# Kernel optimization log

Measured on AMD Instinct MI355X. Metric: run time of the kernel, lower is better.

## Reference

```python
import jax, jax.numpy as jnp
import numpy as np

B, T, D = 64, 4096, 100   # batch, tokens, token_dim == code_dim
K = 4                     # discrete_size: codebook entries
BETA = 0.25               # commitment loss weight


def setup_inputs() -> dict:
    key = jax.random.key(0)
    k_x, k_w, k_b, k_c = jax.random.split(key, 4)
    x = jax.random.normal(k_x, (B, T, D), dtype=jnp.float32)
    W1 = jax.random.normal(k_w, (D, D), dtype=jnp.float32) * (1.0 / np.sqrt(D))
    b1 = jax.random.normal(k_b, (D,), dtype=jnp.float32) * 0.01
    codebook = jax.random.normal(k_c, (K, D), dtype=jnp.float32)
    return {"x": x, "W1": W1, "b1": b1, "codebook": codebook, "quantize": 1}


def reference(x, W1, b1, codebook, quantize):
    # Linear1: Linear(100,100) + ReLU (torch Linear: x @ W.T + b)
    h = jax.nn.relu(jnp.einsum("btd,ed->bte", x, W1) + b1)  # [B,T,D]
    if not quantize:
        return (h, 0, 0, 0)
    # quantizer.compress: VQ-style cdist/argmin/straight-through/loss
    flat = h.reshape(-1, D)  # [N,D]
    d2 = (jnp.sum(flat * flat, axis=-1, keepdims=True)
          - 2.0 * flat @ codebook.T
          + jnp.sum(codebook * codebook, axis=-1))
    idx = jnp.argmin(d2, axis=-1)          # [N] nearest code indices
    q = codebook[idx]                       # [N,D] gathered codes
    sg = jax.lax.stop_gradient
    # codebook loss + commitment loss
    vq_loss = (jnp.mean((sg(flat) - q) ** 2)
               + BETA * jnp.mean((flat - sg(q)) ** 2))
    # straight-through quantized output
    aux = (flat + sg(q - flat)).reshape(B, T, D)
    payload = idx.reshape(B, T)
    return (h, payload, aux, vq_loss)
```

## Files before the change

kernel.cpp:

```cpp
#include <hip/hip_runtime.h>

#define D_DIM   100
#define K_CODES 4
#define RPB     64
#define TPB     256
#define PITCH   65
#define N_ROWS  262144
#define KP      128
#define NP      128
#define TAU     0.25

typedef __attribute__((ext_vector_type(8))) __bf16 bf16x8;
typedef __attribute__((ext_vector_type(4))) float  f32x4;

__device__ __forceinline__ unsigned short f2bf_rne(float f) {
    unsigned int u = __builtin_bit_cast(unsigned int, f);
    unsigned int r = u + 0x7fffu + ((u >> 16) & 1u);
    return (unsigned short)(r >> 16);
}
__device__ __forceinline__ float bf2f(unsigned short b) {
    unsigned int u = ((unsigned int)b) << 16;
    return __builtin_bit_cast(float, u);
}

__device__ __forceinline__ void load_lds16(const float* g, float* s) {
    __builtin_amdgcn_global_load_lds(
        (const __attribute__((address_space(1))) unsigned int*)g,
        (__attribute__((address_space(3))) unsigned int*)s, 16, 0, 0);
}

__global__ __launch_bounds__(256) void split_w_kernel(
    const float* __restrict__ W1,
    unsigned short* __restrict__ Whi, unsigned short* __restrict__ Wlo)
{
    int i = blockIdx.x * 256 + threadIdx.x;
    if (i >= NP * KP) return;
    int n = i / KP, k = i % KP;
    float w = (n < D_DIM && k < D_DIM) ? W1[n * D_DIM + k] : 0.0f;
    unsigned short hb = f2bf_rne(w);
    float lo = w - bf2f(hb);
    Whi[i] = hb;
    Wlo[i] = f2bf_rne(lo);
}

__global__ __launch_bounds__(TPB, 4) void gemm_relu_mfma(
    const float* __restrict__ x,
    const unsigned short* __restrict__ Whi, const unsigned short* __restrict__ Wlo,
    const float* __restrict__ b1, float* __restrict__ out_h)
{
    __shared__ __align__(16) float smem[6500];
    const int tid  = threadIdx.x;
    const int lane = tid & 63;
    const int wave = tid >> 6;
    const int rowBase = blockIdx.x * RPB;
    const float* xg = x + (size_t)rowBase * D_DIM;

    const int bcol0 = wave * 32;
    const int bn  = lane & 15;
    const int bk  = (lane >> 4) * 8;
    bf16x8 bh[2][4], bl[2][4];
    #pragma unroll
    for (int ct = 0; ct < 2; ++ct) {
        int n = bcol0 + ct * 16 + bn;
        #pragma unroll
        for (int kt = 0; kt < 4; ++kt) {
            int off = n * KP + kt * 32 + bk;
            bh[ct][kt] = *reinterpret_cast<const bf16x8*>(Whi + off);
            bl[ct][kt] = *reinterpret_cast<const bf16x8*>(Wlo + off);
        }
    }
    float bias[2];
    #pragma unroll
    for (int ct = 0; ct < 2; ++ct) {
        int n = bcol0 + ct * 16 + bn;
        bias[ct] = (n < D_DIM) ? b1[n] : 0.0f;
    }

    #pragma unroll
    for (int it = 0; it < 6; ++it) {
        int cbase = it * 256 + wave * 64;
        load_lds16(xg + (size_t)(cbase + lane) * 4, smem + cbase * 4);
    }
    if (wave == 0) {
        int cbase = 1536;
        load_lds16(xg + (size_t)(cbase + lane) * 4, smem + cbase * 4);
    }
    if (tid < 32) smem[6400 + tid] = 0.0f;
    __syncthreads();

    const int am = lane & 15;
    const int ak = (lane >> 4) * 8;
    f32x4 acc[4][2];
    #pragma unroll
    for (int rt = 0; rt < 4; ++rt) {
        acc[rt][0] = (f32x4){0.f, 0.f, 0.f, 0.f};
        acc[rt][1] = (f32x4){0.f, 0.f, 0.f, 0.f};
    }
    #pragma unroll
    for (int rt = 0; rt < 4; ++rt) {
        const int rbase = (rt * 16 + am) * D_DIM;
        #pragma unroll
        for (int kt = 0; kt < 4; ++kt) {
            const float* p = smem + rbase + kt * 32 + ak;
            f32x4 f0 = *reinterpret_cast<const f32x4*>(p);
            f32x4 f1 = *reinterpret_cast<const f32x4*>(p + 4);
            bf16x8 ah, al;
            #pragma unroll
            for (int i = 0; i < 4; ++i) {
                __bf16 h0 = (__bf16)f0[i];
                ah[i] = h0;
                al[i] = (__bf16)(f0[i] - (float)h0);
                __bf16 h1 = (__bf16)f1[i];
                ah[4 + i] = h1;
                al[4 + i] = (__bf16)(f1[i] - (float)h1);
            }
            acc[rt][0] = __builtin_amdgcn_mfma_f32_16x16x32_bf16(ah, bl[0][kt], acc[rt][0], 0, 0, 0);
            acc[rt][0] = __builtin_amdgcn_mfma_f32_16x16x32_bf16(al, bh[0][kt], acc[rt][0], 0, 0, 0);
            acc[rt][0] = __builtin_amdgcn_mfma_f32_16x16x32_bf16(ah, bh[0][kt], acc[rt][0], 0, 0, 0);
            acc[rt][1] = __builtin_amdgcn_mfma_f32_16x16x32_bf16(ah, bl[1][kt], acc[rt][1], 0, 0, 0);
            acc[rt][1] = __builtin_amdgcn_mfma_f32_16x16x32_bf16(al, bh[1][kt], acc[rt][1], 0, 0, 0);
            acc[rt][1] = __builtin_amdgcn_mfma_f32_16x16x32_bf16(ah, bh[1][kt], acc[rt][1], 0, 0, 0);
        }
    }
    __syncthreads();

    #pragma unroll
    for (int rt = 0; rt < 4; ++rt) {
        int rb = rt * 16 + (lane >> 4) * 4;
        #pragma unroll
        for (int ct = 0; ct < 2; ++ct) {
            int n = bcol0 + ct * 16 + bn;
            if (n < D_DIM) {
                #pragma unroll
                for (int i = 0; i < 4; ++i)
                    smem[n * PITCH + rb + i] = fmaxf(acc[rt][ct][i] + bias[ct], 0.0f);
            }
        }
    }
    __syncthreads();

    float* hg = out_h + (size_t)rowBase * D_DIM;
    for (int v = tid; v < RPB * 25; v += TPB) {
        int r = v / 25;
        int d = (v % 25) * 4;
        reinterpret_cast<float4*>(hg)[v] = make_float4(
            smem[d * PITCH + r], smem[(d + 1) * PITCH + r],
            smem[(d + 2) * PITCH + r], smem[(d + 3) * PITCH + r]);
    }
}

__global__ __launch_bounds__(TPB) void vq_kernel(
    const float* __restrict__ h, const float* __restrict__ x,
    const float* __restrict__ W1, const float* __restrict__ b1,
    const float* __restrict__ cb, const int* __restrict__ qflag,
    float* __restrict__ out_pay, float* __restrict__ out_aux,
    double* __restrict__ partials)
{
    __shared__ float  tile[D_DIM][PITCH];
    __shared__ double d2s[K_CODES][RPB];
    __shared__ int    idxs[RPB];
    __shared__ unsigned long long flagmask;
    const int tid  = threadIdx.x;
    const int lane = tid & 63;
    const int wave = tid >> 6;
    const int blk  = blockIdx.x;
    const int rowBase = blk * RPB;
    const int qz = *qflag;

    if (qz) {
        const float* hgc = h + (size_t)rowBase * D_DIM;
        for (int v = tid; v < (RPB * D_DIM) / 4; v += TPB) {
            float4 val = reinterpret_cast<const float4*>(hgc)[v];
            int r = v / 25;
            int d = (v % 25) * 4;
            tile[d + 0][r] = val.x; tile[d + 1][r] = val.y;
            tile[d + 2][r] = val.z; tile[d + 3][r] = val.w;
        }
        __syncthreads();
        {
            const int k = __builtin_amdgcn_readfirstlane(wave & 3);
            const float* crow = cb + k * D_DIM;
            double s = 0.0;
            #pragma unroll
            for (int d = 0; d < D_DIM; ++d) {
                double dh = (double)tile[d][lane] - (double)crow[d];
                s = fma(dh, dh, s);
            }
            d2s[k][lane] = s;
        }
        __syncthreads();

        if (wave == 0) {
            double best = d2s[0][lane], second = 1e300;
            int bi = 0;
            #pragma unroll
            for (int k = 1; k < K_CODES; ++k) {
                double v = d2s[k][lane];
                if (v < best) { second = best; best = v; bi = k; }
                else if (v < second) { second = v; }
            }
            idxs[lane] = bi;
            unsigned long long m = __ballot((second - best) < TAU);
            if (lane == 0) flagmask = m;
        }
        __syncthreads();

        {
            unsigned long long m = flagmask;
            int i = 0;
            while (m) {
                int r = __ffsll((long long)m) - 1;
                m &= m - 1;
                if ((i & 3) == wave) {
                    const int e1 = lane;
                    const int e2 = 64 + lane;
                    const bool has2 = (e2 < D_DIM);
                    float z1 = b1[e1];
                    float z2 = has2 ? b1[e2] : 0.0f;
                    const float* xr  = x + (size_t)(rowBase + r) * D_DIM;
                    const float* w1r = W1 + e1 * D_DIM;
                    const float* w2r = W1 + (has2 ? e2 : 0) * D_DIM;
                    #pragma unroll
                    for (int d4 = 0; d4 < 25; ++d4) {
                        float4 xv = reinterpret_cast<const float4*>(xr)[d4];
                        float4 wa = reinterpret_cast<const float4*>(w1r)[d4];
                        z1 = fmaf(xv.x, wa.x, z1); z1 = fmaf(xv.y, wa.y, z1);
                        z1 = fmaf(xv.z, wa.z, z1); z1 = fmaf(xv.w, wa.w, z1);
                        float4 wb = reinterpret_cast<const float4*>(w2r)[d4];
                        z2 = fmaf(xv.x, wb.x, z2); z2 = fmaf(xv.y, wb.y, z2);
                        z2 = fmaf(xv.z, wb.z, z2); z2 = fmaf(xv.w, wb.w, z2);
                    }
                    float h1 = fmaxf(z1, 0.0f);
                    float h2 = fmaxf(z2, 0.0f);
                    double dk[K_CODES];
                    #pragma unroll
                    for (int k = 0; k < K_CODES; ++k) {
                        double p;
                        {
                            double dh = (double)h1 - (double)cb[k * D_DIM + e1];
                            p = dh * dh;
                        }
                        if (has2) {
                            double dh = (double)h2 - (double)cb[k * D_DIM + e2];
                            p = fma(dh, dh, p);
                        }
                        for (int off = 32; off > 0; off >>= 1)
                            p += __shfl_down(p, off);
                        dk[k] = p;
                    }
                    if (lane == 0) {
                        double best = dk[0];
                        int bi = 0;
                        #pragma unroll
                        for (int k = 1; k < K_CODES; ++k)
                            if (dk[k] < best) { best = dk[k]; bi = k; }
                        idxs[r] = bi;
                    }
                }
                ++i;
            }
        }
        __syncthreads();

        if (wave == 0) {
            int bi = idxs[lane];
            out_pay[rowBase + lane] = (float)bi;
            double d2min = d2s[bi][lane];
            for (int off = 32; off > 0; off >>= 1)
                d2min += __shfl_down(d2min, off);
            if (lane == 0) partials[blk] = d2min;
        }

        float* ag = out_aux + (size_t)rowBase * D_DIM;
        for (int v = tid; v < (RPB * D_DIM) / 4; v += TPB) {
            int r = v / 25;
            int d = (v % 25) * 4;
            int bi = idxs[r];
            reinterpret_cast<float4*>(ag)[v] =
                reinterpret_cast<const float4*>(cb + bi * D_DIM + d)[0];
        }
    } else {
        if (wave == 0) {
            out_pay[rowBase + lane] = 0.0f;
            if (lane == 0) partials[blk] = 0.0;
        }
        float* ag = out_aux + (size_t)rowBase * D_DIM;
        for (int v = tid; v < (RPB * D_DIM) / 4; v += TPB)
            reinterpret_cast<float4*>(ag)[v] = make_float4(0, 0, 0, 0);
    }
}

__global__ __launch_bounds__(256) void vq_final_kernel(
    const double* __restrict__ partials, int n, float* __restrict__ loss_out)
{
    __shared__ double sm[256];
    int tid = threadIdx.x;
    double s = 0.0;
    for (int i = tid; i < n; i += 256) s += partials[i];
    sm[tid] = s;
    __syncthreads();
    for (int off = 128; off > 0; off >>= 1) {
        if (tid < off) sm[tid] += sm[tid + off];
        __syncthreads();
    }
    if (tid == 0) {
        double mse = sm[0] / ((double)N_ROWS * (double)D_DIM);
        loss_out[0] = (float)(1.25 * mse);
    }
}

extern "C" void kernel_launch(void* const* d_in, const int* in_sizes, int n_in,
                              void* d_out, int out_size, void* d_ws, size_t ws_size,
                              hipStream_t stream) {
    const float* x  = (const float*)d_in[0];
    const float* W1 = (const float*)d_in[1];
    const float* b1 = (const float*)d_in[2];
    const float* cb = (const float*)d_in[3];
    const int* qflag = (const int*)d_in[4];

    float* out = (float*)d_out;
    const int NR = in_sizes[0] / D_DIM;
    const int nblocks = NR / RPB;

    float* out_h    = out;
    float* out_pay  = out + (size_t)NR * D_DIM;
    float* out_aux  = out_pay + NR;
    float* out_loss = out_aux + (size_t)NR * D_DIM;

    double* partials = (double*)d_ws;
    const size_t w_off = (size_t)nblocks * sizeof(double);
    unsigned short* Whi = (unsigned short*)((char*)d_ws + w_off);
    unsigned short* Wlo = Whi + NP * KP;

    split_w_kernel<<<(NP * KP) / 256, 256, 0, stream>>>(W1, Whi, Wlo);
    gemm_relu_mfma<<<nblocks, TPB, 0, stream>>>(x, Whi, Wlo, b1, out_h);
    vq_kernel<<<nblocks, TPB, 0, stream>>>(out_h, x, W1, b1, cb, qflag,
                                           out_pay, out_aux, partials);
    vq_final_kernel<<<1, 256, 0, stream>>>(partials, nblocks, out_loss);
}
```

Baseline: 127.4 us.

## Make GEMM kernel persistent with double-buffered LDS prefetch of x tiles

The GEMM+ReLU kernel now runs a fixed grid of 1024 blocks, each handling 4 row tiles. While the MFMA work runs on the current tile, it prefetches the next tile of x into a second LDS buffer using global_load_lds. This amortizes the per-block load of the split bf16 weights and bias, and lets the x load overlap compute. The cost is doubled LDS per block, which lowers occupancy. The __syncthreads barriers likely also drain the outstanding async loads partway through each iteration, so the overlap may be limited.

```diff
diff --git a/kernel.cpp b/kernel.cpp
--- a/kernel.cpp
+++ b/kernel.cpp
@@ -9,6 +9,8 @@
 #define KP      128
 #define NP      128
 #define TAU     0.25
+#define GRID_GEMM 1024
+#define NTILES  4
 
 typedef __attribute__((ext_vector_type(8))) __bf16 bf16x8;
 typedef __attribute__((ext_vector_type(4))) float  f32x4;
@@ -27,6 +29,15 @@
     __builtin_amdgcn_global_load_lds(
         (const __attribute__((address_space(1))) unsigned int*)g,
         (__attribute__((address_space(3))) unsigned int*)s, 16, 0, 0);
+}
+
+__device__ __forceinline__ void stage_x(const float* xg, float* s, int wave, int lane) {
+    #pragma unroll
+    for (int it = 0; it < 6; ++it) {
+        int cbase = it * 256 + wave * 64;
+        load_lds16(xg + (size_t)(cbase + lane) * 4, s + cbase * 4);
+    }
+    if (wave == 0) load_lds16(xg + (size_t)(1536 + lane) * 4, s + 1536 * 4);
 }
 
 __global__ __launch_bounds__(256) void split_w_kernel(
@@ -48,12 +59,11 @@
     const unsigned short* __restrict__ Whi, const unsigned short* __restrict__ Wlo,
     const float* __restrict__ b1, float* __restrict__ out_h)
 {
-    __shared__ __align__(16) float smem[6500];
+    __shared__ __align__(16) float buf0[6500];
+    __shared__ __align__(16) float buf1[6500];
     const int tid  = threadIdx.x;
     const int lane = tid & 63;
     const int wave = tid >> 6;
-    const int rowBase = blockIdx.x * RPB;
-    const float* xg = x + (size_t)rowBase * D_DIM;
 
     const int bcol0 = wave * 32;
     const int bn  = lane & 15;
@@ -76,76 +86,82 @@
         bias[ct] = (n < D_DIM) ? b1[n] : 0.0f;
     }
 
-    #pragma unroll
-    for (int it = 0; it < 6; ++it) {
-        int cbase = it * 256 + wave * 64;
-        load_lds16(xg + (size_t)(cbase + lane) * 4, smem + cbase * 4);
-    }
-    if (wave == 0) {
-        int cbase = 1536;
-        load_lds16(xg + (size_t)(cbase + lane) * 4, smem + cbase * 4);
-    }
-    if (tid < 32) smem[6400 + tid] = 0.0f;
-    __syncthreads();
+    if (tid < 32) { buf0[6400 + tid] = 0.0f; buf1[6400 + tid] = 0.0f; }
+
+    stage_x(x + (size_t)blockIdx.x * RPB * D_DIM, buf0, wave, lane);
 
     const int am = lane & 15;
     const int ak = (lane >> 4) * 8;
-    f32x4 acc[4][2];
-    #pragma unroll
-    for (int rt = 0; rt < 4; ++rt) {
-        acc[rt][0] = (f32x4){0.f, 0.f, 0.f, 0.f};
-        acc[rt][1] = (f32x4){0.f, 0.f, 0.f, 0.f};
-    }
-    #pragma unroll
-    for (int rt = 0; rt < 4; ++rt) {
-        const int rbase = (rt * 16 + am) * D_DIM;
+
+    for (int it = 0; it < NTILES; ++it) {
+        const int tile = blockIdx.x + it * GRID_GEMM;
+        const int rowBase = tile * RPB;
+        float* cur = (it & 1) ? buf1 : buf0;
+        float* nxt = (it & 1) ? buf0 : buf1;
+
+        __syncthreads();
+
+        if (it + 1 < NTILES)
+            stage_x(x + (size_t)(blockIdx.x + (it + 1) * GRID_GEMM) * RPB * D_DIM,
+                    nxt, wave, lane);
+
+        f32x4 acc[4][2];
         #pragma unroll
-        for (int kt = 0; kt < 4; ++kt) {
-            const float* p = smem + rbase + kt * 32 + ak;
-            f32x4 f0 = *reinterpret_cast<const f32x4*>(p);
-            f32x4 f1 = *reinterpret_cast<const f32x4*>(p + 4);
-            bf16x8 ah, al;
+        for (int rt = 0; rt < 4; ++rt) {
+            acc[rt][0] = (f32x4){0.f, 0.f, 0.f, 0.f};
+            acc[rt][1] = (f32x4){0.f, 0.f, 0.f, 0.f};
+        }
+        #pragma unroll
+        for (int rt = 0; rt < 4; ++rt) {
+            const int rbase = (rt * 16 + am) * D_DIM;
             #pragma unroll
-            for (int i = 0; i < 4; ++i) {
-                __bf16 h0 = (__bf16)f0[i];
-                ah[i] = h0;
-                al[i] = (__bf16)(f0[i] - (float)h0);
-                __bf16 h1 = (__bf16)f1[i];
-                ah[4 + i] = h1;
-                al[4 + i] = (__bf16)(f1[i] - (float)h1);
-            }
-            acc[rt][0] = __builtin_amdgcn_mfma_f32_16x16x32_bf16(ah, bl[0][kt], acc[rt][0], 0, 0, 0);
-            acc[rt][0] = __builtin_amdgcn_mfma_f32_16x16x32_bf16(al, bh[0][kt], acc[rt][0], 0, 0, 0);
-            acc[rt][0] = __builtin_amdgcn_mfma_f32_16x16x32_bf16(ah, bh[0][kt], acc[rt][0], 0, 0, 0);
-            acc[rt][1] = __builtin_amdgcn_mfma_f32_16x16x32_bf16(ah, bl[1][kt], acc[rt][1], 0, 0, 0);
-            acc[rt][1] = __builtin_amdgcn_mfma_f32_16x16x32_bf16(al, bh[1][kt], acc[rt][1], 0, 0, 0);
-            acc[rt][1] = __builtin_amdgcn_mfma_f32_16x16x32_bf16(ah, bh[1][kt], acc[rt][1], 0, 0, 0);
-        }
-    }
-    __syncthreads();
-
-    #pragma unroll
-    for (int rt = 0; rt < 4; ++rt) {
-        int rb = rt * 16 + (lane >> 4) * 4;
+            for (int kt = 0; kt < 4; ++kt) {
+                const float* p = cur + rbase + kt * 32 + ak;
+                f32x4 f0 = *reinterpret_cast<const f32x4*>(p);
+                f32x4 f1 = *reinterpret_cast<const f32x4*>(p + 4);
+                bf16x8 ah, al;
+                #pragma unroll
+                for (int i = 0; i < 4; ++i) {
+                    __bf16 h0 = (__bf16)f0[i];
+                    ah[i] = h0;
+                    al[i] = (__bf16)(f0[i] - (float)h0);
+                    __bf16 h1 = (__bf16)f1[i];
+                    ah[4 + i] = h1;
+                    al[4 + i] = (__bf16)(f1[i] - (float)h1);
+                }
+                acc[rt][0] = __builtin_amdgcn_mfma_f32_16x16x32_bf16(ah, bl[0][kt], acc[rt][0], 0, 0, 0);
+                acc[rt][0] = __builtin_amdgcn_mfma_f32_16x16x32_bf16(al, bh[0][kt], acc[rt][0], 0, 0, 0);
+                acc[rt][0] = __builtin_amdgcn_mfma_f32_16x16x32_bf16(ah, bh[0][kt], acc[rt][0], 0, 0, 0);
+                acc[rt][1] = __builtin_amdgcn_mfma_f32_16x16x32_bf16(ah, bl[1][kt], acc[rt][1], 0, 0, 0);
+                acc[rt][1] = __builtin_amdgcn_mfma_f32_16x16x32_bf16(al, bh[1][kt], acc[rt][1], 0, 0, 0);
+                acc[rt][1] = __builtin_amdgcn_mfma_f32_16x16x32_bf16(ah, bh[1][kt], acc[rt][1], 0, 0, 0);
+            }
+        }
+        __syncthreads();
+
         #pragma unroll
-        for (int ct = 0; ct < 2; ++ct) {
-            int n = bcol0 + ct * 16 + bn;
-            if (n < D_DIM) {
-                #pragma unroll
-                for (int i = 0; i < 4; ++i)
-                    smem[n * PITCH + rb + i] = fmaxf(acc[rt][ct][i] + bias[ct], 0.0f);
-            }
-        }
-    }
-    __syncthreads();
-
-    float* hg = out_h + (size_t)rowBase * D_DIM;
-    for (int v = tid; v < RPB * 25; v += TPB) {
-        int r = v / 25;
-        int d = (v % 25) * 4;
-        reinterpret_cast<float4*>(hg)[v] = make_float4(
-            smem[d * PITCH + r], smem[(d + 1) * PITCH + r],
-            smem[(d + 2) * PITCH + r], smem[(d + 3) * PITCH + r]);
+        for (int rt = 0; rt < 4; ++rt) {
+            int rb = rt * 16 + (lane >> 4) * 4;
+            #pragma unroll
+            for (int ct = 0; ct < 2; ++ct) {
+                int n = bcol0 + ct * 16 + bn;
+                if (n < D_DIM) {
+                    #pragma unroll
+                    for (int i = 0; i < 4; ++i)
+                        cur[n * PITCH + rb + i] = fmaxf(acc[rt][ct][i] + bias[ct], 0.0f);
+                }
+            }
+        }
+        __syncthreads();
+
+        float* hg = out_h + (size_t)rowBase * D_DIM;
+        for (int v = tid; v < RPB * 25; v += TPB) {
+            int r = v / 25;
+            int d = (v % 25) * 4;
+            reinterpret_cast<float4*>(hg)[v] = make_float4(
+                cur[d * PITCH + r], cur[(d + 1) * PITCH + r],
+                cur[(d + 2) * PITCH + r], cur[(d + 3) * PITCH + r]);
+        }
     }
 }
 
@@ -333,7 +349,7 @@
     unsigned short* Wlo = Whi + NP * KP;
 
     split_w_kernel<<<(NP * KP) / 256, 256, 0, stream>>>(W1, Whi, Wlo);
-    gemm_relu_mfma<<<nblocks, TPB, 0, stream>>>(x, Whi, Wlo, b1, out_h);
+    gemm_relu_mfma<<<GRID_GEMM, TPB, 0, stream>>>(x, Whi, Wlo, b1, out_h);
     vq_kernel<<<nblocks, TPB, 0, stream>>>(out_h, x, W1, b1, cb, qflag,
                                            out_pay, out_aux, partials);
     vq_final_kernel<<<1, 256, 0, stream>>>(partials, nblocks, out_loss);
```

After: 117.6 us. 7.7% less time.

## Fuse GEMM+ReLU and VQ into one persistent kernel over row tiles

Applied to the files above, without the earlier changes.

Merges the GEMM+ReLU kernel and the VQ kernel into one kernel, so the h tile stays in LDS and is no longer re-read from global memory for the distance computation. The grid becomes a fixed 1024 blocks, each looping over four 64-row tiles. This also reuses the per-block W fragments loaded into registers across tiles. The cost is that the per-tile stages (load, MFMA, VQ, stores) now run serially inside each block, with no overlap between them. The tile count is hard-coded and assumes exactly 4096 tiles.

```diff
diff --git a/kernel.cpp b/kernel.cpp
--- a/kernel.cpp
+++ b/kernel.cpp
@@ -9,6 +9,8 @@
 #define KP      128
 #define NP      128
 #define TAU     0.25
+#define GRID_GEMM 1024
+#define NTILES  4
 
 typedef __attribute__((ext_vector_type(8))) __bf16 bf16x8;
 typedef __attribute__((ext_vector_type(4))) float  f32x4;
@@ -27,6 +29,15 @@
     __builtin_amdgcn_global_load_lds(
         (const __attribute__((address_space(1))) unsigned int*)g,
         (__attribute__((address_space(3))) unsigned int*)s, 16, 0, 0);
+}
+
+__device__ __forceinline__ void stage_x(const float* xg, float* s, int wave, int lane) {
+    #pragma unroll
+    for (int it = 0; it < 6; ++it) {
+        int cbase = it * 256 + wave * 64;
+        load_lds16(xg + (size_t)(cbase + lane) * 4, s + cbase * 4);
+    }
+    if (wave == 0) load_lds16(xg + (size_t)(1536 + lane) * 4, s + 1536 * 4);
 }
 
 __global__ __launch_bounds__(256) void split_w_kernel(
@@ -43,17 +54,23 @@
     Wlo[i] = f2bf_rne(lo);
 }
 
-__global__ __launch_bounds__(TPB, 4) void gemm_relu_mfma(
+__global__ __launch_bounds__(TPB, 4) void fused_kernel(
     const float* __restrict__ x,
     const unsigned short* __restrict__ Whi, const unsigned short* __restrict__ Wlo,
-    const float* __restrict__ b1, float* __restrict__ out_h)
+    const float* __restrict__ b1, const float* __restrict__ cb,
+    const float* __restrict__ W1, const int* __restrict__ qflag,
+    float* __restrict__ out_h, float* __restrict__ out_pay,
+    float* __restrict__ out_aux, double* __restrict__ partials)
 {
     __shared__ __align__(16) float smem[6500];
+    __shared__ double d2s[K_CODES][RPB];
+    __shared__ int    idxs[RPB];
+    __shared__ unsigned long long flagmask;
+
     const int tid  = threadIdx.x;
     const int lane = tid & 63;
     const int wave = tid >> 6;
-    const int rowBase = blockIdx.x * RPB;
-    const float* xg = x + (size_t)rowBase * D_DIM;
+    const int qz = *qflag;
 
     const int bcol0 = wave * 32;
     const int bn  = lane & 15;
@@ -75,218 +92,192 @@
         int n = bcol0 + ct * 16 + bn;
         bias[ct] = (n < D_DIM) ? b1[n] : 0.0f;
     }
-
-    #pragma unroll
-    for (int it = 0; it < 6; ++it) {
-        int cbase = it * 256 + wave * 64;
-        load_lds16(xg + (size_t)(cbase + lane) * 4, smem + cbase * 4);
-    }
-    if (wave == 0) {
-        int cbase = 1536;
-        load_lds16(xg + (size_t)(cbase + lane) * 4, smem + cbase * 4);
-    }
     if (tid < 32) smem[6400 + tid] = 0.0f;
-    __syncthreads();
 
     const int am = lane & 15;
     const int ak = (lane >> 4) * 8;
-    f32x4 acc[4][2];
-    #pragma unroll
-    for (int rt = 0; rt < 4; ++rt) {
-        acc[rt][0] = (f32x4){0.f, 0.f, 0.f, 0.f};
-        acc[rt][1] = (f32x4){0.f, 0.f, 0.f, 0.f};
-    }
-    #pragma unroll
-    for (int rt = 0; rt < 4; ++rt) {
-        const int rbase = (rt * 16 + am) * D_DIM;
+
+    for (int it = 0; it < NTILES; ++it) {
+        const int tile = blockIdx.x + it * GRID_GEMM;
+        const int rowBase = tile * RPB;
+        const float* xg = x + (size_t)rowBase * D_DIM;
+
+        __syncthreads();
+        stage_x(xg, smem, wave, lane);
+        __syncthreads();
+
+        f32x4 acc[4][2];
         #pragma unroll
-        for (int kt = 0; kt < 4; ++kt) {
-            const float* p = smem + rbase + kt * 32 + ak;
-            f32x4 f0 = *reinterpret_cast<const f32x4*>(p);
-            f32x4 f1 = *reinterpret_cast<const f32x4*>(p + 4);
-            bf16x8 ah, al;
+        for (int rt = 0; rt < 4; ++rt) {
+            acc[rt][0] = (f32x4){0.f, 0.f, 0.f, 0.f};
+            acc[rt][1] = (f32x4){0.f, 0.f, 0.f, 0.f};
+        }
+        #pragma unroll
+        for (int rt = 0; rt < 4; ++rt) {
+            const int rbase = (rt * 16 + am) * D_DIM;
             #pragma unroll
-            for (int i = 0; i < 4; ++i) {
-                __bf16 h0 = (__bf16)f0[i];
-                ah[i] = h0;
-                al[i] = (__bf16)(f0[i] - (float)h0);
-                __bf16 h1 = (__bf16)f1[i];
-                ah[4 + i] = h1;
-                al[4 + i] = (__bf16)(f1[i] - (float)h1);
-            }
-            acc[rt][0] = __builtin_amdgcn_mfma_f32_16x16x32_bf16(ah, bl[0][kt], acc[rt][0], 0, 0, 0);
-            acc[rt][0] = __builtin_amdgcn_mfma_f32_16x16x32_bf16(al, bh[0][kt], acc[rt][0], 0, 0, 0);
-            acc[rt][0] = __builtin_amdgcn_mfma_f32_16x16x32_bf16(ah, bh[0][kt], acc[rt][0], 0, 0, 0);
-            acc[rt][1] = __builtin_amdgcn_mfma_f32_16x16x32_bf16(ah, bl[1][kt], acc[rt][1], 0, 0, 0);
-            acc[rt][1] = __builtin_amdgcn_mfma_f32_16x16x32_bf16(al, bh[1][kt], acc[rt][1], 0, 0, 0);
-            acc[rt][1] = __builtin_amdgcn_mfma_f32_16x16x32_bf16(ah, bh[1][kt], acc[rt][1], 0, 0, 0);
-        }
-    }
-    __syncthreads();
-
-    #pragma unroll
-    for (int rt = 0; rt < 4; ++rt) {
-        int rb = rt * 16 + (lane >> 4) * 4;
+            for (int kt = 0; kt < 4; ++kt) {
+                const float* p = smem + rbase + kt * 32 + ak;
+                f32x4 f0 = *reinterpret_cast<const f32x4*>(p);
+                f32x4 f1 = *reinterpret_cast<const f32x4*>(p + 4);
+                bf16x8 ah, al;
+                #pragma unroll
+                for (int i = 0; i < 4; ++i) {
+                    __bf16 h0 = (__bf16)f0[i];
+                    ah[i] = h0;
+                    al[i] = (__bf16)(f0[i] - (float)h0);
+                    __bf16 h1 = (__bf16)f1[i];
+                    ah[4 + i] = h1;
+                    al[4 + i] = (__bf16)(f1[i] - (float)h1);
+                }
+                acc[rt][0] = __builtin_amdgcn_mfma_f32_16x16x32_bf16(ah, bl[0][kt], acc[rt][0], 0, 0, 0);
+                acc[rt][0] = __builtin_amdgcn_mfma_f32_16x16x32_bf16(al, bh[0][kt], acc[rt][0], 0, 0, 0);
+                acc[rt][0] = __builtin_amdgcn_mfma_f32_16x16x32_bf16(ah, bh[0][kt], acc[rt][0], 0, 0, 0);
+                acc[rt][1] = __builtin_amdgcn_mfma_f32_16x16x32_bf16(ah, bl[1][kt], acc[rt][1], 0, 0, 0);
+                acc[rt][1] = __builtin_amdgcn_mfma_f32_16x16x32_bf16(al, bh[1][kt], acc[rt][1], 0, 0, 0);
+                acc[rt][1] = __builtin_amdgcn_mfma_f32_16x16x32_bf16(ah, bh[1][kt], acc[rt][1], 0, 0, 0);
+            }
+        }
+        __syncthreads();
+
         #pragma unroll
-        for (int ct = 0; ct < 2; ++ct) {
-            int n = bcol0 + ct * 16 + bn;
-            if (n < D_DIM) {
+        for (int rt = 0; rt < 4; ++rt) {
+            int rb = rt * 16 + (lane >> 4) * 4;
+            #pragma unroll
+            for (int ct = 0; ct < 2; ++ct) {
+                int n = bcol0 + ct * 16 + bn;
+                if (n < D_DIM) {
+                    #pragma unroll
+                    for (int i = 0; i < 4; ++i)
+                        smem[n * PITCH + rb + i] = fmaxf(acc[rt][ct][i] + bias[ct], 0.0f);
+                }
+            }
+        }
+        __syncthreads();
+
+        if (qz) {
+            {
+                const int k = __builtin_amdgcn_readfirstlane(wave & 3);
+                const float* crow = cb + k * D_DIM;
+                double s = 0.0;
                 #pragma unroll
-                for (int i = 0; i < 4; ++i)
-                    smem[n * PITCH + rb + i] = fmaxf(acc[rt][ct][i] + bias[ct], 0.0f);
-            }
-        }
-    }
-    __syncthreads();
-
-    float* hg = out_h + (size_t)rowBase * D_DIM;
-    for (int v = tid; v < RPB * 25; v += TPB) {
-        int r = v / 25;
-        int d = (v % 25) * 4;
-        reinterpret_cast<float4*>(hg)[v] = make_float4(
-            smem[d * PITCH + r], smem[(d + 1) * PITCH + r],
-            smem[(d + 2) * PITCH + r], smem[(d + 3) * PITCH + r]);
-    }
-}
-
-__global__ __launch_bounds__(TPB) void vq_kernel(
-    const float* __restrict__ h, const float* __restrict__ x,
-    const float* __restrict__ W1, const float* __restrict__ b1,
-    const float* __restrict__ cb, const int* __restrict__ qflag,
-    float* __restrict__ out_pay, float* __restrict__ out_aux,
-    double* __restrict__ partials)
-{
-    __shared__ float  tile[D_DIM][PITCH];
-    __shared__ double d2s[K_CODES][RPB];
-    __shared__ int    idxs[RPB];
-    __shared__ unsigned long long flagmask;
-    const int tid  = threadIdx.x;
-    const int lane = tid & 63;
-    const int wave = tid >> 6;
-    const int blk  = blockIdx.x;
-    const int rowBase = blk * RPB;
-    const int qz = *qflag;
-
-    if (qz) {
-        const float* hgc = h + (size_t)rowBase * D_DIM;
-        for (int v = tid; v < (RPB * D_DIM) / 4; v += TPB) {
-            float4 val = reinterpret_cast<const float4*>(hgc)[v];
-            int r = v / 25;
-            int d = (v % 25) * 4;
-            tile[d + 0][r] = val.x; tile[d + 1][r] = val.y;
-            tile[d + 2][r] = val.z; tile[d + 3][r] = val.w;
-        }
-        __syncthreads();
-        {
-            const int k = __builtin_amdgcn_readfirstlane(wave & 3);
-            const float* crow = cb + k * D_DIM;
-            double s = 0.0;
-            #pragma unroll
-            for (int d = 0; d < D_DIM; ++d) {
-                double dh = (double)tile[d][lane] - (double)crow[d];
-                s = fma(dh, dh, s);
-            }
-            d2s[k][lane] = s;
-        }
-        __syncthreads();
-
-        if (wave == 0) {
-            double best = d2s[0][lane], second = 1e300;
-            int bi = 0;
-            #pragma unroll
-            for (int k = 1; k < K_CODES; ++k) {
-                double v = d2s[k][lane];
-                if (v < best) { second = best; best = v; bi = k; }
-                else if (v < second) { second = v; }
-            }
-            idxs[lane] = bi;
-            unsigned long long m = __ballot((second - best) < TAU);
-            if (lane == 0) flagmask = m;
-        }
-        __syncthreads();
-
-        {
-            unsigned long long m = flagmask;
-            int i = 0;
-            while (m) {
-                int r = __ffsll((long long)m) - 1;
-                m &= m - 1;
-                if ((i & 3) == wave) {
-                    const int e1 = lane;
-                    const int e2 = 64 + lane;
-                    const bool has2 = (e2 < D_DIM);
-                    float z1 = b1[e1];
-                    float z2 = has2 ? b1[e2] : 0.0f;
-                    const float* xr  = x + (size_t)(rowBase + r) * D_DIM;
-                    const float* w1r = W1 + e1 * D_DIM;
-                    const float* w2r = W1 + (has2 ? e2 : 0) * D_DIM;
-                    #pragma unroll
-                    for (int d4 = 0; d4 < 25; ++d4) {
-                        float4 xv = reinterpret_cast<const float4*>(xr)[d4];
-                        float4 wa = reinterpret_cast<const float4*>(w1r)[d4];
-                        z1 = fmaf(xv.x, wa.x, z1); z1 = fmaf(xv.y, wa.y, z1);
-                        z1 = fmaf(xv.z, wa.z, z1); z1 = fmaf(xv.w, wa.w, z1);
-                        float4 wb = reinterpret_cast<const float4*>(w2r)[d4];
-                        z2 = fmaf(xv.x, wb.x, z2); z2 = fmaf(xv.y, wb.y, z2);
-                        z2 = fmaf(xv.z, wb.z, z2); z2 = fmaf(xv.w, wb.w, z2);
+                for (int d = 0; d < D_DIM; ++d) {
+                    double dh = (double)smem[d * PITCH + lane] - (double)crow[d];
+                    s = fma(dh, dh, s);
+                }
+                d2s[k][lane] = s;
+            }
+            __syncthreads();
+
+            if (wave == 0) {
+                double best = d2s[0][lane], second = 1e300;
+                int bi = 0;
+                #pragma unroll
+                for (int k = 1; k < K_CODES; ++k) {
+                    double v = d2s[k][lane];
+                    if (v < best) { second = best; best = v; bi = k; }
+                    else if (v < second) { second = v; }
+                }
+                idxs[lane] = bi;
+                unsigned long long m = __ballot((second - best) < TAU);
+                if (lane == 0) flagmask = m;
+            }
+            __syncthreads();
+
+            {
+                unsigned long long m = flagmask;
+                int i = 0;
+                while (m) {
+                    int r = __ffsll((long long)m) - 1;
+                    m &= m - 1;
+                    if ((i & 3) == wave) {
+                        const int e1 = lane;
+                        const int e2 = 64 + lane;
+                        const bool has2 = (e2 < D_DIM);
+                        float z1 = b1[e1];
+                        float z2 = has2 ? b1[e2] : 0.0f;
+                        const float* xr  = x + (size_t)(rowBase + r) * D_DIM;
+                        const float* w1r = W1 + e1 * D_DIM;
+                        const float* w2r = W1 + (has2 ? e2 : 0) * D_DIM;
+                        #pragma unroll
+                        for (int d4 = 0; d4 < 25; ++d4) {
+                            float4 xv = reinterpret_cast<const float4*>(xr)[d4];
+                            float4 wa = reinterpret_cast<const float4*>(w1r)[d4];
+                            z1 = fmaf(xv.x, wa.x, z1); z1 = fmaf(xv.y, wa.y, z1);
+                            z1 = fmaf(xv.z, wa.z, z1); z1 = fmaf(xv.w, wa.w, z1);
+                            float4 wb = reinterpret_cast<const float4*>(w2r)[d4];
+                            z2 = fmaf(xv.x, wb.x, z2); z2 = fmaf(xv.y, wb.y, z2);
+                            z2 = fmaf(xv.z, wb.z, z2); z2 = fmaf(xv.w, wb.w, z2);
+                        }
+                        float h1 = fmaxf(z1, 0.0f);
+                        float h2 = fmaxf(z2, 0.0f);
+                        double dk[K_CODES];
+                        #pragma unroll
+                        for (int k = 0; k < K_CODES; ++k) {
+                            double p;
+                            {
+                                double dh = (double)h1 - (double)cb[k * D_DIM + e1];
+                                p = dh * dh;
+                            }
+                            if (has2) {
+                                double dh = (double)h2 - (double)cb[k * D_DIM + e2];
+                                p = fma(dh, dh, p);
+                            }
+                            for (int off = 32; off > 0; off >>= 1)
+                                p += __shfl_down(p, off);
+                            dk[k] = p;
+                        }
+                        if (lane == 0) {
+                            double best = dk[0];
+                            int bi = 0;
+                            #pragma unroll
+                            for (int k = 1; k < K_CODES; ++k)
+                                if (dk[k] < best) { best = dk[k]; bi = k; }
+                            idxs[r] = bi;
+                        }
                     }
-                    float h1 = fmaxf(z1, 0.0f);
-                    float h2 = fmaxf(z2, 0.0f);
-                    double dk[K_CODES];
-                    #pragma unroll
-                    for (int k = 0; k < K_CODES; ++k) {
-                        double p;
-                        {
-                            double dh = (double)h1 - (double)cb[k * D_DIM + e1];
-                            p = dh * dh;
-                        }
-                        if (has2) {
-                            double dh = (double)h2 - (double)cb[k * D_DIM + e2];
-                            p = fma(dh, dh, p);
-                        }
-                        for (int off = 32; off > 0; off >>= 1)
-                            p += __shfl_down(p, off);
-                        dk[k] = p;
-                    }
-                    if (lane == 0) {
-                        double best = dk[0];
-                        int bi = 0;
-                        #pragma unroll
-                        for (int k = 1; k < K_CODES; ++k)
-                            if (dk[k] < best) { best = dk[k]; bi = k; }
-                        idxs[r] = bi;
-                    }
-                }
-                ++i;
-            }
-        }
-        __syncthreads();
-
-        if (wave == 0) {
-            int bi = idxs[lane];
-            out_pay[rowBase + lane] = (float)bi;
-            double d2min = d2s[bi][lane];
-            for (int off = 32; off > 0; off >>= 1)
-                d2min += __shfl_down(d2min, off);
-            if (lane == 0) partials[blk] = d2min;
-        }
-
-        float* ag = out_aux + (size_t)rowBase * D_DIM;
-        for (int v = tid; v < (RPB * D_DIM) / 4; v += TPB) {
-            int r = v / 25;
-            int d = (v % 25) * 4;
-            int bi = idxs[r];
-            reinterpret_cast<float4*>(ag)[v] =
-                reinterpret_cast<const float4*>(cb + bi * D_DIM + d)[0];
-        }
-    } else {
-        if (wave == 0) {
-            out_pay[rowBase + lane] = 0.0f;
-            if (lane == 0) partials[blk] = 0.0;
-        }
-        float* ag = out_aux + (size_t)rowBase * D_DIM;
-        for (int v = tid; v < (RPB * D_DIM) / 4; v += TPB)
-            reinterpret_cast<float4*>(ag)[v] = make_float4(0, 0, 0, 0);
+                    ++i;
+                }
+            }
+            __syncthreads();
+
+            if (wave == 0) {
+                int bi = idxs[lane];
+                out_pay[rowBase + lane] = (float)bi;
+                double d2min = d2s[bi][lane];
+                for (int off = 32; off > 0; off >>= 1)
+                    d2min += __shfl_down(d2min, off);
+                if (lane == 0) partials[tile] = d2min;
+            }
+
+            float* hg = out_h + (size_t)rowBase * D_DIM;
+            float* ag = out_aux + (size_t)rowBase * D_DIM;
+            for (int v = tid; v < RPB * 25; v += TPB) {
+                int r = v / 25;
+                int d = (v % 25) * 4;
+                reinterpret_cast<float4*>(hg)[v] = make_float4(
+                    smem[d * PITCH + r], smem[(d + 1) * PITCH + r],
+                    smem[(d + 2) * PITCH + r], smem[(d + 3) * PITCH + r]);
+                int bi = idxs[r];
+                reinterpret_cast<float4*>(ag)[v] =
+                    reinterpret_cast<const float4*>(cb + bi * D_DIM + d)[0];
+            }
+        } else {
+            if (wave == 0) {
+                out_pay[rowBase + lane] = 0.0f;
+                if (lane == 0) partials[tile] = 0.0;
+            }
+            float* hg = out_h + (size_t)rowBase * D_DIM;
+            float* ag = out_aux + (size_t)rowBase * D_DIM;
+            for (int v = tid; v < RPB * 25; v += TPB) {
+                int r = v / 25;
+                int d = (v % 25) * 4;
+                reinterpret_cast<float4*>(hg)[v] = make_float4(
+                    smem[d * PITCH + r], smem[(d + 1) * PITCH + r],
+                    smem[(d + 2) * PITCH + r], smem[(d + 3) * PITCH + r]);
+                reinterpret_cast<float4*>(ag)[v] = make_float4(0, 0, 0, 0);
+            }
+        }
     }
 }
 
@@ -333,8 +324,7 @@
     unsigned short* Wlo = Whi + NP * KP;
 
     split_w_kernel<<<(NP * KP) / 256, 256, 0, stream>>>(W1, Whi, Wlo);
-    gemm_relu_mfma<<<nblocks, TPB, 0, stream>>>(x, Whi, Wlo, b1, out_h);
-    vq_kernel<<<nblocks, TPB, 0, stream>>>(out_h, x, W1, b1, cb, qflag,
-                                           out_pay, out_aux, partials);
+    fused_kernel<<<GRID_GEMM, TPB, 0, stream>>>(x, Whi, Wlo, b1, cb, W1, qflag,
+                                                out_h, out_pay, out_aux, partials);
     vq_final_kernel<<<1, 256, 0, stream>>>(partials, nblocks, out_loss);
 }
```

Result: slower. 201.9 us (+58.5%).

## Fuse weight split into persistent GEMM with swizzled LDS weights and direct loads

Applied to the files above, without the earlier changes.

Removes the separate weight-split kernel; each 512-thread block now converts W1 to hi/lo bf16 into an XOR-swizzled LDS buffer once. A fixed grid of blocks is launched, and each wave processes 4 row tiles of 16. A operands are loaded straight from global memory into registers instead of being staged in LDS, and outputs are written directly from MFMA accumulators as scattered strided stores instead of going through an LDS transpose. This saves a launch and LDS staging, but each block redundantly recomputes the weight split, and the output stores are uncoalesced.

```diff
diff --git a/kernel.cpp b/kernel.cpp
--- a/kernel.cpp
+++ b/kernel.cpp
@@ -6,9 +6,11 @@
 #define TPB     256
 #define PITCH   65
 #define N_ROWS  262144
-#define KP      128
-#define NP      128
 #define TAU     0.25
+#define GEMM_TPB 512
+#define GEMM_GRID 512
+#define TILES_PER_WAVE 4
+#define NB_PAD  112
 
 typedef __attribute__((ext_vector_type(8))) __bf16 bf16x8;
 typedef __attribute__((ext_vector_type(4))) float  f32x4;
@@ -23,129 +25,102 @@
     return __builtin_bit_cast(float, u);
 }
 
-__device__ __forceinline__ void load_lds16(const float* g, float* s) {
-    __builtin_amdgcn_global_load_lds(
-        (const __attribute__((address_space(1))) unsigned int*)g,
-        (__attribute__((address_space(3))) unsigned int*)s, 16, 0, 0);
-}
-
-__global__ __launch_bounds__(256) void split_w_kernel(
-    const float* __restrict__ W1,
-    unsigned short* __restrict__ Whi, unsigned short* __restrict__ Wlo)
-{
-    int i = blockIdx.x * 256 + threadIdx.x;
-    if (i >= NP * KP) return;
-    int n = i / KP, k = i % KP;
-    float w = (n < D_DIM && k < D_DIM) ? W1[n * D_DIM + k] : 0.0f;
-    unsigned short hb = f2bf_rne(w);
-    float lo = w - bf2f(hb);
-    Whi[i] = hb;
-    Wlo[i] = f2bf_rne(lo);
-}
-
-__global__ __launch_bounds__(TPB, 4) void gemm_relu_mfma(
-    const float* __restrict__ x,
-    const unsigned short* __restrict__ Whi, const unsigned short* __restrict__ Wlo,
+__global__ __launch_bounds__(GEMM_TPB, 4) void gemm_relu_mfma(
+    const float* __restrict__ x, const float* __restrict__ W1,
     const float* __restrict__ b1, float* __restrict__ out_h)
 {
-    __shared__ __align__(16) float smem[6500];
+    __shared__ unsigned short Bhi[NB_PAD * 128];
+    __shared__ unsigned short Blo[NB_PAD * 128];
     const int tid  = threadIdx.x;
     const int lane = tid & 63;
     const int wave = tid >> 6;
-    const int rowBase = blockIdx.x * RPB;
-    const float* xg = x + (size_t)rowBase * D_DIM;
-
-    const int bcol0 = wave * 32;
-    const int bn  = lane & 15;
-    const int bk  = (lane >> 4) * 8;
-    bf16x8 bh[2][4], bl[2][4];
+    const int rw = lane & 15;
+    const int kp = lane >> 4;
+
+    for (int i = tid; i < NB_PAD * 128; i += GEMM_TPB) {
+        int n = i >> 7, k = i & 127;
+        float w = (n < D_DIM && k < D_DIM) ? W1[n * D_DIM + k] : 0.0f;
+        unsigned short hb = f2bf_rne(w);
+        unsigned short lb = f2bf_rne(w - bf2f(hb));
+        int byte = (n * 256 + k * 2) ^ ((n & 7) << 4);
+        *reinterpret_cast<unsigned short*>(reinterpret_cast<char*>(Bhi) + byte) = hb;
+        *reinterpret_cast<unsigned short*>(reinterpret_cast<char*>(Blo) + byte) = lb;
+    }
+
+    float bias[7];
     #pragma unroll
-    for (int ct = 0; ct < 2; ++ct) {
-        int n = bcol0 + ct * 16 + bn;
+    for (int ct = 0; ct < 7; ++ct) {
+        int n = ct * 16 + rw;
+        bias[ct] = (n < D_DIM) ? b1[n] : 0.0f;
+    }
+
+    __syncthreads();
+
+    const int wg = blockIdx.x * 8 + wave;
+
+    #pragma unroll
+    for (int t = 0; t < TILES_PER_WAVE; ++t) {
+        const int tile = wg + t * 4096;
+        const float* base = x + (size_t)tile * 16 * D_DIM + rw * D_DIM;
+
+        f32x4 f0[4], f1[4];
+        #pragma unroll
+        for (int kt = 0; kt < 3; ++kt) {
+            const float* p = base + kt * 32 + kp * 8;
+            f0[kt] = *reinterpret_cast<const f32x4*>(p);
+            f1[kt] = *reinterpret_cast<const f32x4*>(p + 4);
+        }
+        if (kp == 0)
+            f0[3] = *reinterpret_cast<const f32x4*>(base + 96);
+        else
+            f0[3] = (f32x4){0.f, 0.f, 0.f, 0.f};
+        f1[3] = (f32x4){0.f, 0.f, 0.f, 0.f};
+
+        bf16x8 ah[4], al[4];
         #pragma unroll
         for (int kt = 0; kt < 4; ++kt) {
-            int off = n * KP + kt * 32 + bk;
-            bh[ct][kt] = *reinterpret_cast<const bf16x8*>(Whi + off);
-            bl[ct][kt] = *reinterpret_cast<const bf16x8*>(Wlo + off);
-        }
-    }
-    float bias[2];
-    #pragma unroll
-    for (int ct = 0; ct < 2; ++ct) {
-        int n = bcol0 + ct * 16 + bn;
-        bias[ct] = (n < D_DIM) ? b1[n] : 0.0f;
-    }
-
-    #pragma unroll
-    for (int it = 0; it < 6; ++it) {
-        int cbase = it * 256 + wave * 64;
-        load_lds16(xg + (size_t)(cbase + lane) * 4, smem + cbase * 4);
-    }
-    if (wave == 0) {
-        int cbase = 1536;
-        load_lds16(xg + (size_t)(cbase + lane) * 4, smem + cbase * 4);
-    }
-    if (tid < 32) smem[6400 + tid] = 0.0f;
-    __syncthreads();
-
-    const int am = lane & 15;
-    const int ak = (lane >> 4) * 8;
-    f32x4 acc[4][2];
-    #pragma unroll
-    for (int rt = 0; rt < 4; ++rt) {
-        acc[rt][0] = (f32x4){0.f, 0.f, 0.f, 0.f};
-        acc[rt][1] = (f32x4){0.f, 0.f, 0.f, 0.f};
-    }
-    #pragma unroll
-    for (int rt = 0; rt < 4; ++rt) {
-        const int rbase = (rt * 16 + am) * D_DIM;
+            #pragma unroll
+            for (int i = 0; i < 4; ++i) {
+                __bf16 h0 = (__bf16)f0[kt][i];
+                ah[kt][i] = h0;
+                al[kt][i] = (__bf16)(f0[kt][i] - (float)h0);
+                __bf16 h1 = (__bf16)f1[kt][i];
+                ah[kt][4 + i] = h1;
+                al[kt][4 + i] = (__bf16)(f1[kt][i] - (float)h1);
+            }
+        }
+
+        const int rb = tile * 16 + kp * 4;
+        const int n =  0;
+        (void)n;
         #pragma unroll
-        for (int kt = 0; kt < 4; ++kt) {
-            const float* p = smem + rbase + kt * 32 + ak;
-            f32x4 f0 = *reinterpret_cast<const f32x4*>(p);
-            f32x4 f1 = *reinterpret_cast<const f32x4*>(p + 4);
-            bf16x8 ah, al;
-            #pragma unroll
-            for (int i = 0; i < 4; ++i) {
-                __bf16 h0 = (__bf16)f0[i];
-                ah[i] = h0;
-                al[i] = (__bf16)(f0[i] - (float)h0);
-                __bf16 h1 = (__bf16)f1[i];
-                ah[4 + i] = h1;
-                al[4 + i] = (__bf16)(f1[i] - (float)h1);
-            }
-            acc[rt][0] = __builtin_amdgcn_mfma_f32_16x16x32_bf16(ah, bl[0][kt], acc[rt][0], 0, 0, 0);
-            acc[rt][0] = __builtin_amdgcn_mfma_f32_16x16x32_bf16(al, bh[0][kt], acc[rt][0], 0, 0, 0);
-            acc[rt][0] = __builtin_amdgcn_mfma_f32_16x16x32_bf16(ah, bh[0][kt], acc[rt][0], 0, 0, 0);
-            acc[rt][1] = __builtin_amdgcn_mfma_f32_16x16x32_bf16(ah, bl[1][kt], acc[rt][1], 0, 0, 0);
-            acc[rt][1] = __builtin_amdgcn_mfma_f32_16x16x32_bf16(al, bh[1][kt], acc[rt][1], 0, 0, 0);
-            acc[rt][1] = __builtin_amdgcn_mfma_f32_16x16x32_bf16(ah, bh[1][kt], acc[rt][1], 0, 0, 0);
-        }
-    }
-    __syncthreads();
-
-    #pragma unroll
-    for (int rt = 0; rt < 4; ++rt) {
-        int rb = rt * 16 + (lane >> 4) * 4;
-        #pragma unroll
-        for (int ct = 0; ct < 2; ++ct) {
-            int n = bcol0 + ct * 16 + bn;
-            if (n < D_DIM) {
+        for (int ct = 0; ct < 7; ++ct) {
+            const int col = ct * 16 + rw;
+            bf16x8 bhf[4], blf[4];
+            #pragma unroll
+            for (int kt = 0; kt < 4; ++kt) {
+                int byte = ((ct * 16 + rw) * 256 + (kt * 32 + kp * 8) * 2)
+                           ^ (((ct * 16 + rw) & 7) << 4);
+                bhf[kt] = *reinterpret_cast<const bf16x8*>(
+                    reinterpret_cast<const char*>(Bhi) + byte);
+                blf[kt] = *reinterpret_cast<const bf16x8*>(
+                    reinterpret_cast<const char*>(Blo) + byte);
+            }
+            f32x4 a = {0.f, 0.f, 0.f, 0.f};
+            #pragma unroll
+            for (int kt = 0; kt < 4; ++kt) {
+                a = __builtin_amdgcn_mfma_f32_16x16x32_bf16(ah[kt], blf[kt], a, 0, 0, 0);
+                a = __builtin_amdgcn_mfma_f32_16x16x32_bf16(al[kt], bhf[kt], a, 0, 0, 0);
+                a = __builtin_amdgcn_mfma_f32_16x16x32_bf16(ah[kt], bhf[kt], a, 0, 0, 0);
+            }
+            if (col < D_DIM) {
                 #pragma unroll
-                for (int i = 0; i < 4; ++i)
-                    smem[n * PITCH + rb + i] = fmaxf(acc[rt][ct][i] + bias[ct], 0.0f);
-            }
-        }
-    }
-    __syncthreads();
-
-    float* hg = out_h + (size_t)rowBase * D_DIM;
-    for (int v = tid; v < RPB * 25; v += TPB) {
-        int r = v / 25;
-        int d = (v % 25) * 4;
-        reinterpret_cast<float4*>(hg)[v] = make_float4(
-            smem[d * PITCH + r], smem[(d + 1) * PITCH + r],
-            smem[(d + 2) * PITCH + r], smem[(d + 3) * PITCH + r]);
+                for (int i = 0; i < 4; ++i) {
+                    float h = fmaxf(a[i] + bias[ct], 0.0f);
+                    out_h[(size_t)(rb + i) * D_DIM + col] = h;
+                }
+            }
+        }
     }
 }
 
@@ -326,14 +301,9 @@
     float* out_pay  = out + (size_t)NR * D_DIM;
     float* out_aux  = out_pay + NR;
     float* out_loss = out_aux + (size_t)NR * D_DIM;
-
     double* partials = (double*)d_ws;
-    const size_t w_off = (size_t)nblocks * sizeof(double);
-    unsigned short* Whi = (unsigned short*)((char*)d_ws + w_off);
-    unsigned short* Wlo = Whi + NP * KP;
-
-    split_w_kernel<<<(NP * KP) / 256, 256, 0, stream>>>(W1, Whi, Wlo);
-    gemm_relu_mfma<<<nblocks, TPB, 0, stream>>>(x, Whi, Wlo, b1, out_h);
+
+    gemm_relu_mfma<<<GEMM_GRID, GEMM_TPB, 0, stream>>>(x, W1, b1, out_h);
     vq_kernel<<<nblocks, TPB, 0, stream>>>(out_h, x, W1, b1, cb, qflag,
                                            out_pay, out_aux, partials);
     vq_final_kernel<<<1, 256, 0, stream>>>(partials, nblocks, out_loss);
```

New measurement: 117.9 us. 7.5% less time.
